# Performance work log

Measured on AMD Instinct MI355X. Metric: run time of the kernel, lower is better.

The kernel has to match this reference:

```python
import jax, jax.numpy as jnp
import numpy as np

# ---------------- geometry constants (from init_kwargs) ----------------
N_PROJ = 96          # cone-beam projections (batch of 2D BP, views of 3D BP)
A2D    = 96          # 2D parallel angles (= detector rows of cone sinogram)
DET2D  = 192         # 2D detector bins   (= detector cols of cone sinogram)
DS2D   = 1.0         # 2D detector spacing
H = 128
W = 128              # intermediate CB_projection image (geom_2d volume)
Zd = 128
Yd = 128
Xd = 128             # reconstruction volume (geometry.volume_shape)
DSO = 500.0          # source-isocenter distance
DSD = 1000.0         # source-detector distance
DU = 3.5
DV = 3.5             # 3D detector spacing (detector grid == H x W image grid)


def _grad_lastdim(x):
    # torch.gradient(x, dim=-1) with unit spacing: central diffs, one-sided edges
    left = x[..., 1:2] - x[..., 0:1]
    mid = (x[..., 2:] - x[..., :-2]) * 0.5
    right = x[..., -1:] - x[..., -2:-1]
    return jnp.concatenate([left, mid, right], axis=-1)


def _image_grid(h, w):
    ys = jnp.arange(h, dtype=jnp.float32) - (h - 1) / 2.0
    xs = jnp.arange(w, dtype=jnp.float32) - (w - 1) / 2.0
    yg, xg = jnp.meshgrid(ys, xs, indexing='ij')  # [h, w]
    return yg, xg


def _weights_3d():
    # Defrise-Clack intermediate-function weighting: cosine of ray angle,
    # w(x,y) = D / sqrt(D^2 + x^2 + y^2) on the intermediate image grid.
    yg, xg = _image_grid(H, W)
    return DSD / jnp.sqrt(DSD * DSD + xg * xg + yg * yg)


def _bp2d(sino):
    # Pixel-driven 2D parallel backprojection, batched over N.
    # sino: [N, A2D, DET2D] -> [N, H, W]
    yg, xg = _image_grid(H, W)
    th = jnp.arange(A2D, dtype=jnp.float32) * (np.pi / A2D)
    s = jnp.cos(th)[:, None, None] * xg + jnp.sin(th)[:, None, None] * yg  # [A,H,W]
    pos = s / DS2D + (DET2D - 1) / 2.0
    i0 = jnp.floor(pos).astype(jnp.int32)
    f = pos - i0
    i1 = i0 + 1
    w0 = jnp.where((i0 >= 0) & (i0 < DET2D), 1.0 - f, 0.0)
    w1 = jnp.where((i1 >= 0) & (i1 < DET2D), f, 0.0)
    i0c = jnp.clip(i0, 0, DET2D - 1)
    i1c = jnp.clip(i1, 0, DET2D - 1)
    aa = jnp.arange(A2D)[:, None, None]  # [A,1,1]
    g0 = sino[:, aa, i0c]  # [N, A, H, W]
    g1 = sino[:, aa, i1c]
    return (g0 * w0 + g1 * w1).sum(axis=1)  # [N, H, W]


def _bp3d(projs):
    # Voxel-driven circular cone-beam backprojection with FDK distance weight.
    # projs: [N_PROJ, H, W] (V=H rows, U=W cols) -> volume [Zd, Yd, Xd]
    zs = jnp.arange(Zd, dtype=jnp.float32) - (Zd - 1) / 2.0
    ys = jnp.arange(Yd, dtype=jnp.float32) - (Yd - 1) / 2.0
    xs = jnp.arange(Xd, dtype=jnp.float32) - (Xd - 1) / 2.0
    zz, yy, xx = jnp.meshgrid(zs, ys, xs, indexing='ij')  # [Z,Y,X]
    betas = jnp.arange(N_PROJ, dtype=jnp.float32) * (2.0 * np.pi / N_PROJ)

    def body(acc, inp):
        beta, proj = inp
        cb, sb = jnp.cos(beta), jnp.sin(beta)
        t = xx * cb + yy * sb          # along central ray
        s = -xx * sb + yy * cb         # transaxial offset
        r = DSO + t                    # source-to-voxel-plane distance
        pu = (DSD * s / r) / DU + (W - 1) / 2.0
        pv = (DSD * zz / r) / DV + (H - 1) / 2.0
        iu0 = jnp.floor(pu).astype(jnp.int32); fu = pu - iu0; iu1 = iu0 + 1
        iv0 = jnp.floor(pv).astype(jnp.int32); fv = pv - iv0; iv1 = iv0 + 1
        mu0 = (iu0 >= 0) & (iu0 < W); mu1 = (iu1 >= 0) & (iu1 < W)
        mv0 = (iv0 >= 0) & (iv0 < H); mv1 = (iv1 >= 0) & (iv1 < H)
        iu0c = jnp.clip(iu0, 0, W - 1); iu1c = jnp.clip(iu1, 0, W - 1)
        iv0c = jnp.clip(iv0, 0, H - 1); iv1c = jnp.clip(iv1, 0, H - 1)
        w00 = jnp.where(mv0 & mu0, (1 - fv) * (1 - fu), 0.0)
        w01 = jnp.where(mv0 & mu1, (1 - fv) * fu, 0.0)
        w10 = jnp.where(mv1 & mu0, fv * (1 - fu), 0.0)
        w11 = jnp.where(mv1 & mu1, fv * fu, 0.0)
        val = (proj[iv0c, iu0c] * w00 + proj[iv0c, iu1c] * w01 +
               proj[iv1c, iu0c] * w10 + proj[iv1c, iu1c] * w11)
        acc = acc + val * (DSD / r) ** 2
        return acc, None

    acc, _ = jax.lax.scan(body, jnp.zeros((Zd, Yd, Xd), jnp.float32), (betas, projs))
    return acc


def setup_inputs() -> dict:
    key = jax.random.key(0)
    k1, k2 = jax.random.split(key)
    sinogram = jax.random.normal(k1, (1, 1, N_PROJ, A2D, DET2D), dtype=jnp.float32)
    weight = jax.random.uniform(k2, (1, N_PROJ, A2D, DET2D), dtype=jnp.float32)
    prelu_weight = jnp.full((1,), 0.25, dtype=jnp.float32)
    return {"sinogram": sinogram, "weight": weight, "prelu_weight": prelu_weight}


def reference(sinogram, weight, prelu_weight):
    ws = sinogram[0] * weight                 # [1, N, A, D]
    deriv = _grad_lastdim(ws)[0]              # [N, A, D]  (squeeze dim 0)
    cb = _bp2d(deriv)                         # [N, H, W]
    weighted_cb = cb * _weights_3d()          # [N, H, W]
    reco = _bp3d(weighted_cb)[None]           # [1, Z, Y, X]
    a = prelu_weight[0]
    return jnp.where(reco >= 0, reco, a * reco)  # PReLU (single parameter)
```

## Files before the change

### kernel.cpp

```cpp
#include <hip/hip_runtime.h>
#include <hip/hip_fp16.h>
#include <math.h>

#define NPROJ 96
#define NANG  96
#define DET   192
#define NPIX  16384
#define SLICE (NANG*DET)

#define KPROJ 285.7142857142857f

__device__ __forceinline__ float frcp(float x) { return __builtin_amdgcn_rcpf(x); }

__device__ __forceinline__ float ffract(float x) {
#if __has_builtin(__builtin_amdgcn_fractf)
    return __builtin_amdgcn_fractf(x);
#else
    return x - floorf(x);
#endif
}

typedef __fp16 h2 __attribute__((ext_vector_type(2)));

__device__ __forceinline__ unsigned pack2(float a, float b) {
    h2 p = __builtin_amdgcn_cvt_pkrtz(a, b);
    return __builtin_bit_cast(unsigned, p);
}
__device__ __forceinline__ h2 as_h2(unsigned u) { return __builtin_bit_cast(h2, u); }

#if __has_builtin(__builtin_amdgcn_fdot2)
#define FDOT2(a, b, c) __builtin_amdgcn_fdot2((a), (b), (c), false)
#else
__device__ __forceinline__ float FDOT2(h2 a, h2 b, float c) {
    return c + (float)a[0] * (float)b[0] + (float)a[1] * (float)b[1];
}
#endif

__global__ __launch_bounds__(192) void k_deriv(const float* __restrict__ sino,
                                               const float* __restrict__ wgt,
                                               unsigned* __restrict__ derivp) {
    __shared__ float row[DET];
    const int r = blockIdx.x;
    const int d = threadIdx.x;
    const int base = r * DET + d;
    row[d] = sino[base] * wgt[base];
    __syncthreads();
    float g0, g1;
    if (d == 0)            g0 = row[1] - row[0];
    else if (d == DET-1)   g0 = row[DET-1] - row[DET-2];
    else                   g0 = 0.5f * (row[d+1] - row[d-1]);
    if (d >= DET-2)        g1 = (d == DET-1) ? 0.0f : row[DET-1] - row[DET-2];
    else                   g1 = 0.5f * (row[d+2] - row[d]);
    derivp[base] = pack2(g0, g1);
}

__global__ __launch_bounds__(256) void k_bp2d(const unsigned* __restrict__ derivp,
                                              unsigned* __restrict__ wcb4) {
    __shared__ float sc[NANG], ss[NANG];
    __shared__ float buf[512];
    const int p   = blockIdx.x;
    const int tid = threadIdx.x;

    if (tid < NANG) {
        float s_, c_;
        sincosf((float)tid * (float)(3.14159265358979323846 / 96.0), &s_, &c_);
        sc[tid] = c_; ss[tid] = s_;
    }

    const int pixbase = blockIdx.y * 512;
    float acc[2], fx[2], fy[2];
    #pragma unroll
    for (int i = 0; i < 2; ++i) {
        const int pix = pixbase + i*256 + tid;
        fx[i] = (float)(pix & 127) - 63.5f;
        fy[i] = (float)(pix >> 7)  - 63.5f;
        acc[i] = 0.0f;
    }
    __syncthreads();

    const unsigned* rowp = derivp + p * SLICE;
    for (int a = 0; a < NANG; ++a, rowp += DET) {
        const float cb = sc[a], sb = ss[a];
        #pragma unroll
        for (int i = 0; i < 2; ++i) {
            const float pos = fmaf(cb, fx[i], fmaf(sb, fy[i], 95.5f));
            const int   i0  = (int)pos;
            const float f   = ffract(pos);
            const h2    g   = as_h2(rowp[i0]);
            acc[i] = FDOT2(g, as_h2(pack2(1.0f - f, f)), acc[i]);
        }
    }

    #pragma unroll
    for (int i = 0; i < 2; ++i) {
        const float w = 1000.0f * rsqrtf(1000000.0f + fx[i]*fx[i] + fy[i]*fy[i]);
        buf[i*256 + tid] = acc[i] * w;
    }
    __syncthreads();
    unsigned* slice4 = wcb4 + p * (NPIX * 2);
    #pragma unroll
    for (int i = 0; i < 2; ++i) {
        const int l   = i*256 + tid;
        const int pix = pixbase + l;
        const int u   = pix & 127;
        const int v   = pix >> 7;
        const float v0 = buf[l];
        const float v1 = (u < 127) ? buf[l + 1] : 0.0f;
        const unsigned pr = pack2(v0, v1);
        slice4[pix * 2] = pr;
        if (v >= 1) slice4[(pix - 128) * 2 + 1] = pr;
    }
}

__global__ __launch_bounds__(256) void k_bp3d(const uint2* __restrict__ wcb4,
                                              const float* __restrict__ prelu,
                                              float* __restrict__ out) {
    __shared__ float sc[NPROJ], ss[NPROJ];
    const int tid = threadIdx.x;
    const int x   = tid & 127;
    const int y   = (blockIdx.x << 1) | (tid >> 7);
    const int z0  = blockIdx.y << 2;

    if (tid < NPROJ) {
        float s_, c_;
        sincosf((float)tid * (float)(2.0 * 3.14159265358979323846 / 96.0), &s_, &c_);
        sc[tid] = c_; ss[tid] = s_;
    }

    const float fx  = (float)x - 63.5f;
    const float fy  = (float)y - 63.5f;
    const float zlo = (float)z0 - 63.5f;

    float acc[4];
    #pragma unroll
    for (int j = 0; j < 4; ++j) acc[j] = 0.0f;

    __syncthreads();

    const uint2* bb = wcb4;
    for (int b = 0; b < NPROJ; ++b, bb += NPIX) {
        const float cb    = sc[b], sb = ss[b];
        const float t     = fmaf(fx, cb,  fy * sb);
        const float sdist = fmaf(fy, cb, -fx * sb);
        const float invr  = frcp(500.0f + t);
        const float pu    = fmaf(KPROJ * sdist, invr, 63.5f);
        const int   iu0   = (int)pu;
        const float fu    = ffract(pu);
        float w2 = 1000.0f * invr; w2 *= w2;
        const float Kz    = KPROJ * invr;
        const h2    wu    = as_h2(pack2(1.0f - fu, fu));

        int   off[4];
        float fv[4];
        #pragma unroll
        for (int j = 0; j < 4; ++j) {
            const float pv  = fmaf(Kz, zlo + (float)j, 63.5f);
            const int   iv0 = (int)pv;
            fv[j]  = ffract(pv);
            off[j] = (iv0 << 7) + iu0;
        }
        uint2 g[4];
        #pragma unroll
        for (int j = 0; j < 4; ++j) g[j] = bb[off[j]];
        #pragma unroll
        for (int j = 0; j < 4; ++j) {
            const float top = FDOT2(as_h2(g[j].x), wu, 0.0f);
            const float bot = FDOT2(as_h2(g[j].y), wu, 0.0f);
            acc[j] = fmaf(fmaf(fv[j], bot - top, top), w2, acc[j]);
        }
    }

    const float a = prelu[0];
    #pragma unroll
    for (int j = 0; j < 4; ++j) {
        const float v = acc[j];
        out[((z0 + j) << 14) + (y << 7) + x] = (v >= 0.0f) ? v : a * v;
    }
}

extern "C" void kernel_launch(void* const* d_in, const int* in_sizes, int n_in,
                              void* d_out, int out_size, void* d_ws, size_t ws_size,
                              hipStream_t stream) {
    const float* sino  = (const float*)d_in[0];
    const float* wgt   = (const float*)d_in[1];
    const float* prelu = (const float*)d_in[2];
    unsigned* derivp = (unsigned*)d_ws;
    unsigned* wcb4   = derivp + NPROJ * SLICE;
    float* out = (float*)d_out;

    k_deriv<<<dim3(NPROJ * NANG), dim3(192), 0, stream>>>(sino, wgt, derivp);
    k_bp2d <<<dim3(NPROJ, 32),    dim3(256), 0, stream>>>(derivp, wcb4);
    k_bp3d <<<dim3(64, 32),       dim3(256), 0, stream>>>((const uint2*)wcb4, prelu, out);
}
```

Measured before the change: 198.8 us.

## Pack row-pair quads for 3D backprojection and pair pixels in 2D backprojection

Changes the intermediate cone-projection layout so each 16-byte entry holds four consecutive detector rows (two row-pairs) as fp16 pairs. In the 3D backprojection two adjacent z-slices can then share one uint4 gather instead of two uint2 gathers. The 2D backprojection now has each thread handle two horizontally adjacent pixels, and the derivative kernel emits a three-sample window so both pixels read one uint2. The cost is more select logic, double the derivative workspace, and a fallback path chosen by workspace size; the layout also assumes two neighbouring z-slices land within a span of four rows.

```diff
diff --git a/kernel.cpp b/kernel.cpp
--- a/kernel.cpp
+++ b/kernel.cpp
@@ -35,6 +35,25 @@
     return c + (float)a[0] * (float)b[0] + (float)a[1] * (float)b[1];
 }
 #endif
+
+__global__ __launch_bounds__(192) void k_deriv2(const float* __restrict__ sino,
+                                                const float* __restrict__ wgt,
+                                                uint2* __restrict__ derivq) {
+    __shared__ float row[DET];
+    const int r = blockIdx.x;
+    const int d = threadIdx.x;
+    const int base = r * DET + d;
+    row[d] = sino[base] * wgt[base];
+    __syncthreads();
+    auto grad = [&](int i) -> float {
+        i = (i > DET-1) ? DET-1 : i;
+        if (i == 0)       return row[1] - row[0];
+        if (i == DET-1)   return row[DET-1] - row[DET-2];
+        return 0.5f * (row[i+1] - row[i-1]);
+    };
+    const float g0 = grad(d), g1 = grad(d+1), g2 = grad(d+2);
+    derivq[base] = make_uint2(pack2(g0, g1), pack2(g1, g2));
+}
 
 __global__ __launch_bounds__(192) void k_deriv(const float* __restrict__ sino,
                                                const float* __restrict__ wgt,
@@ -45,74 +64,114 @@
     const int base = r * DET + d;
     row[d] = sino[base] * wgt[base];
     __syncthreads();
-    float g0, g1;
-    if (d == 0)            g0 = row[1] - row[0];
-    else if (d == DET-1)   g0 = row[DET-1] - row[DET-2];
-    else                   g0 = 0.5f * (row[d+1] - row[d-1]);
-    if (d >= DET-2)        g1 = (d == DET-1) ? 0.0f : row[DET-1] - row[DET-2];
-    else                   g1 = 0.5f * (row[d+2] - row[d]);
-    derivp[base] = pack2(g0, g1);
-}
-
-__global__ __launch_bounds__(256) void k_bp2d(const unsigned* __restrict__ derivp,
-                                              unsigned* __restrict__ wcb4) {
-    __shared__ float sc[NANG], ss[NANG];
-    __shared__ float buf[512];
-    const int p   = blockIdx.x;
-    const int tid = threadIdx.x;
-
-    if (tid < NANG) {
-        float s_, c_;
-        sincosf((float)tid * (float)(3.14159265358979323846 / 96.0), &s_, &c_);
-        sc[tid] = c_; ss[tid] = s_;
-    }
-
-    const int pixbase = blockIdx.y * 512;
-    float acc[2], fx[2], fy[2];
+    auto grad = [&](int i) -> float {
+        i = (i > DET-1) ? DET-1 : i;
+        if (i == 0)       return row[1] - row[0];
+        if (i == DET-1)   return row[DET-1] - row[DET-2];
+        return 0.5f * (row[i+1] - row[i-1]);
+    };
+    derivp[base] = pack2(grad(d), grad(d+1));
+}
+
+__device__ __forceinline__ void bp2d_epilogue(float* buf, int tid, int pixbase,
+                                              int p, unsigned* wcbq_dw) {
+    __syncthreads();
+    unsigned* sq = wcbq_dw + p * 32768;
     #pragma unroll
     for (int i = 0; i < 2; ++i) {
-        const int pix = pixbase + i*256 + tid;
-        fx[i] = (float)(pix & 127) - 63.5f;
-        fy[i] = (float)(pix >> 7)  - 63.5f;
-        acc[i] = 0.0f;
-    }
-    __syncthreads();
-
-    const unsigned* rowp = derivp + p * SLICE;
-    for (int a = 0; a < NANG; ++a, rowp += DET) {
-        const float cb = sc[a], sb = ss[a];
-        #pragma unroll
-        for (int i = 0; i < 2; ++i) {
-            const float pos = fmaf(cb, fx[i], fmaf(sb, fy[i], 95.5f));
-            const int   i0  = (int)pos;
-            const float f   = ffract(pos);
-            const h2    g   = as_h2(rowp[i0]);
-            acc[i] = FDOT2(g, as_h2(pack2(1.0f - f, f)), acc[i]);
-        }
-    }
-
-    #pragma unroll
-    for (int i = 0; i < 2; ++i) {
-        const float w = 1000.0f * rsqrtf(1000000.0f + fx[i]*fx[i] + fy[i]*fy[i]);
-        buf[i*256 + tid] = acc[i] * w;
-    }
-    __syncthreads();
-    unsigned* slice4 = wcb4 + p * (NPIX * 2);
-    #pragma unroll
-    for (int i = 0; i < 2; ++i) {
-        const int l   = i*256 + tid;
+        const int l   = 2*tid + i;
         const int pix = pixbase + l;
         const int u   = pix & 127;
         const int v   = pix >> 7;
         const float v0 = buf[l];
         const float v1 = (u < 127) ? buf[l + 1] : 0.0f;
         const unsigned pr = pack2(v0, v1);
-        slice4[pix * 2] = pr;
-        if (v >= 1) slice4[(pix - 128) * 2 + 1] = pr;
-    }
-}
-
-__global__ __launch_bounds__(256) void k_bp3d(const uint2* __restrict__ wcb4,
+        const int vq1 = v >> 1, k1 = v & 1;
+        sq[(((vq1 << 7) + u) << 2) + k1] = pr;
+        const int vq2 = vq1 - 1;
+        if (vq2 >= 0) sq[(((vq2 << 7) + u) << 2) + k1 + 2] = pr;
+    }
+}
+
+__global__ __launch_bounds__(256) void k_bp2d_pair(const uint2* __restrict__ derivq,
+                                                   unsigned* __restrict__ wcbq_dw) {
+    __shared__ float sc[NANG], ss[NANG];
+    __shared__ float buf[512];
+    const int p   = blockIdx.x;
+    const int tid = threadIdx.x;
+
+    if (tid < NANG) {
+        float s_, c_;
+        sincosf((float)tid * (float)(3.14159265358979323846 / 96.0), &s_, &c_);
+        sc[tid] = c_; ss[tid] = s_;
+    }
+
+    const int pixbase = blockIdx.y * 512;
+    const int px0 = pixbase + 2*tid;
+    const float fx0 = (float)(px0 & 127) - 63.5f;
+    const float fy  = (float)(px0 >> 7)  - 63.5f;
+    float acc0 = 0.0f, acc1 = 0.0f;
+    __syncthreads();
+
+    const uint2* rowq = derivq + p * SLICE;
+    for (int a = 0; a < NANG; ++a, rowq += DET) {
+        const float cb = sc[a], sb = ss[a];
+        const float pos0 = fmaf(cb, fx0, fmaf(sb, fy, 95.5f));
+        const float pos1 = pos0 + cb;
+        const int i0 = (int)pos0;
+        const int i1 = (int)pos1;
+        const int m  = (i0 < i1) ? i0 : i1;
+        const uint2 q = rowq[m];
+        const unsigned pa = (i0 == m) ? q.x : q.y;
+        const unsigned pb = (i1 == m) ? q.x : q.y;
+        const float f0 = ffract(pos0);
+        const float f1 = ffract(pos1);
+        acc0 = FDOT2(as_h2(pa), as_h2(pack2(1.0f - f0, f0)), acc0);
+        acc1 = FDOT2(as_h2(pb), as_h2(pack2(1.0f - f1, f1)), acc1);
+    }
+
+    const float fx1 = fx0 + 1.0f;
+    buf[2*tid]     = acc0 * (1000.0f * rsqrtf(1000000.0f + fx0*fx0 + fy*fy));
+    buf[2*tid + 1] = acc1 * (1000.0f * rsqrtf(1000000.0f + fx1*fx1 + fy*fy));
+    bp2d_epilogue(buf, tid, pixbase, p, wcbq_dw);
+}
+
+__global__ __launch_bounds__(256) void k_bp2d_fb(const unsigned* __restrict__ derivp,
+                                                 unsigned* __restrict__ wcbq_dw) {
+    __shared__ float sc[NANG], ss[NANG];
+    __shared__ float buf[512];
+    const int p   = blockIdx.x;
+    const int tid = threadIdx.x;
+    if (tid < NANG) {
+        float s_, c_;
+        sincosf((float)tid * (float)(3.14159265358979323846 / 96.0), &s_, &c_);
+        sc[tid] = c_; ss[tid] = s_;
+    }
+    const int pixbase = blockIdx.y * 512;
+    const int px0 = pixbase + 2*tid;
+    const float fx0 = (float)(px0 & 127) - 63.5f;
+    const float fy  = (float)(px0 >> 7)  - 63.5f;
+    float acc0 = 0.0f, acc1 = 0.0f;
+    __syncthreads();
+    const unsigned* rowp = derivp + p * SLICE;
+    for (int a = 0; a < NANG; ++a, rowp += DET) {
+        const float cb = sc[a], sb = ss[a];
+        const float pos0 = fmaf(cb, fx0, fmaf(sb, fy, 95.5f));
+        const float pos1 = pos0 + cb;
+        const int i0 = (int)pos0;
+        const int i1 = (int)pos1;
+        const float f0 = ffract(pos0);
+        const float f1 = ffract(pos1);
+        acc0 = FDOT2(as_h2(rowp[i0]), as_h2(pack2(1.0f - f0, f0)), acc0);
+        acc1 = FDOT2(as_h2(rowp[i1]), as_h2(pack2(1.0f - f1, f1)), acc1);
+    }
+    const float fx1 = fx0 + 1.0f;
+    buf[2*tid]     = acc0 * (1000.0f * rsqrtf(1000000.0f + fx0*fx0 + fy*fy));
+    buf[2*tid + 1] = acc1 * (1000.0f * rsqrtf(1000000.0f + fx1*fx1 + fy*fy));
+    bp2d_epilogue(buf, tid, pixbase, p, wcbq_dw);
+}
+
+__global__ __launch_bounds__(256) void k_bp3d(const uint4* __restrict__ wcbq,
                                               const float* __restrict__ prelu,
                                               float* __restrict__ out) {
     __shared__ float sc[NPROJ], ss[NPROJ];
@@ -137,8 +196,8 @@
 
     __syncthreads();
 
-    const uint2* bb = wcb4;
-    for (int b = 0; b < NPROJ; ++b, bb += NPIX) {
+    const uint4* bb = wcbq;
+    for (int b = 0; b < NPROJ; ++b, bb += 8192) {
         const float cb    = sc[b], sb = ss[b];
         const float t     = fmaf(fx, cb,  fy * sb);
         const float sdist = fmaf(fy, cb, -fx * sb);
@@ -150,23 +209,28 @@
         const float Kz    = KPROJ * invr;
         const h2    wu    = as_h2(pack2(1.0f - fu, fu));
 
-        int   off[4];
-        float fv[4];
         #pragma unroll
-        for (int j = 0; j < 4; ++j) {
-            const float pv  = fmaf(Kz, zlo + (float)j, 63.5f);
-            const int   iv0 = (int)pv;
-            fv[j]  = ffract(pv);
-            off[j] = (iv0 << 7) + iu0;
-        }
-        uint2 g[4];
-        #pragma unroll
-        for (int j = 0; j < 4; ++j) g[j] = bb[off[j]];
-        #pragma unroll
-        for (int j = 0; j < 4; ++j) {
-            const float top = FDOT2(as_h2(g[j].x), wu, 0.0f);
-            const float bot = FDOT2(as_h2(g[j].y), wu, 0.0f);
-            acc[j] = fmaf(fmaf(fv[j], bot - top, top), w2, acc[j]);
+        for (int pr2 = 0; pr2 < 2; ++pr2) {
+            const float pvA = fmaf(Kz, zlo + (float)(2*pr2),     63.5f);
+            const float pvB = fmaf(Kz, zlo + (float)(2*pr2 + 1), 63.5f);
+            const int   ivA = (int)pvA;
+            const int   ivB = (int)pvB;
+            const float fvA = ffract(pvA);
+            const float fvB = ffract(pvB);
+            const int   bqi = ivA >> 1;
+            const int   s   = ivA & 1;
+            const int   dS  = ivB - (bqi << 1);
+            const uint4 q   = bb[(bqi << 7) + iu0];
+            const unsigned topA = s ? q.y : q.x;
+            const unsigned botA = s ? q.z : q.y;
+            unsigned topB = (dS >= 1) ? q.y : q.x;  topB = (dS >= 2) ? q.z : topB;
+            unsigned botB = (dS >= 1) ? q.z : q.y;  botB = (dS >= 2) ? q.w : botB;
+            const float tA = FDOT2(as_h2(topA), wu, 0.0f);
+            const float bA = FDOT2(as_h2(botA), wu, 0.0f);
+            acc[2*pr2]     = fmaf(fmaf(fvA, bA - tA, tA), w2, acc[2*pr2]);
+            const float tB = FDOT2(as_h2(topB), wu, 0.0f);
+            const float bB = FDOT2(as_h2(botB), wu, 0.0f);
+            acc[2*pr2 + 1] = fmaf(fmaf(fvB, bB - tB, tB), w2, acc[2*pr2 + 1]);
         }
     }
 
@@ -184,11 +248,19 @@
     const float* sino  = (const float*)d_in[0];
     const float* wgt   = (const float*)d_in[1];
     const float* prelu = (const float*)d_in[2];
-    unsigned* derivp = (unsigned*)d_ws;
-    unsigned* wcb4   = derivp + NPROJ * SLICE;
     float* out = (float*)d_out;
 
-    k_deriv<<<dim3(NPROJ * NANG), dim3(192), 0, stream>>>(sino, wgt, derivp);
-    k_bp2d <<<dim3(NPROJ, 32),    dim3(256), 0, stream>>>(derivp, wcb4);
-    k_bp3d <<<dim3(64, 32),       dim3(256), 0, stream>>>((const uint2*)wcb4, prelu, out);
-}
+    const size_t wcbq_bytes = (size_t)NPROJ * 64 * 128 * 16;
+    unsigned* wcbq_dw = (unsigned*)d_ws;
+    char*     deriv_p = (char*)d_ws + wcbq_bytes;
+    const size_t need_primary = wcbq_bytes + (size_t)NPROJ * SLICE * 8;
+
+    if (ws_size >= need_primary) {
+        k_deriv2<<<dim3(NPROJ * NANG), dim3(192), 0, stream>>>(sino, wgt, (uint2*)deriv_p);
+        k_bp2d_pair<<<dim3(NPROJ, 32), dim3(256), 0, stream>>>((const uint2*)deriv_p, wcbq_dw);
+    } else {
+        k_deriv<<<dim3(NPROJ * NANG), dim3(192), 0, stream>>>(sino, wgt, (unsigned*)deriv_p);
+        k_bp2d_fb<<<dim3(NPROJ, 32), dim3(256), 0, stream>>>((const unsigned*)deriv_p, wcbq_dw);
+    }
+    k_bp3d<<<dim3(64, 32), dim3(256), 0, stream>>>((const uint4*)wcbq_dw, prelu, out);
+}
```

Result: slower. 220.0 us (+10.7%).

## Store four-row packed fp16 quads so 3D backprojection fetches two z-samples per load

Applied to the files above, without the earlier changes.

The 2D backprojection now writes each intermediate pixel pair into a 4-row interleaved layout (16 bytes per texel), so one uint4 load in the 3D backprojection covers the rows needed for two adjacent z voxels. The per-projection weight w2 is folded into the packed u-interpolation weights, which removes one multiply per voxel. The quad layout doubles the intermediate buffer and its write traffic, and it assumes adjacent z samples never differ by more than one detector row. A fallback path keeps the old 2-row layout when workspace is too small.

```diff
diff --git a/kernel.cpp b/kernel.cpp
--- a/kernel.cpp
+++ b/kernel.cpp
@@ -54,8 +54,9 @@
     derivp[base] = pack2(g0, g1);
 }
 
-__global__ __launch_bounds__(256) void k_bp2d(const unsigned* __restrict__ derivp,
-                                              unsigned* __restrict__ wcb4) {
+template <int QUAD>
+__global__ __launch_bounds__(256) void k_bp2d_t(const unsigned* __restrict__ derivp,
+                                                unsigned* __restrict__ dst) {
     __shared__ float sc[NANG], ss[NANG];
     __shared__ float buf[512];
     const int p   = blockIdx.x;
@@ -97,7 +98,6 @@
         buf[i*256 + tid] = acc[i] * w;
     }
     __syncthreads();
-    unsigned* slice4 = wcb4 + p * (NPIX * 2);
     #pragma unroll
     for (int i = 0; i < 2; ++i) {
         const int l   = i*256 + tid;
@@ -107,14 +107,24 @@
         const float v0 = buf[l];
         const float v1 = (u < 127) ? buf[l + 1] : 0.0f;
         const unsigned pr = pack2(v0, v1);
-        slice4[pix * 2] = pr;
-        if (v >= 1) slice4[(pix - 128) * 2 + 1] = pr;
-    }
-}
-
-__global__ __launch_bounds__(256) void k_bp3d(const uint2* __restrict__ wcb4,
-                                              const float* __restrict__ prelu,
-                                              float* __restrict__ out) {
+        if (QUAD) {
+            unsigned* sq = dst + p * (NPIX * 4);
+            #pragma unroll
+            for (int k = 0; k < 4; ++k) {
+                const int vb = v - k;
+                if (vb >= 0) sq[(((vb << 7) + u) << 2) + k] = pr;
+            }
+        } else {
+            unsigned* s2 = dst + p * (NPIX * 2);
+            s2[pix * 2] = pr;
+            if (v >= 1) s2[(pix - 128) * 2 + 1] = pr;
+        }
+    }
+}
+
+__global__ __launch_bounds__(256) void k_bp3d_q(const uint4* __restrict__ wq,
+                                                const float* __restrict__ prelu,
+                                                float* __restrict__ out) {
     __shared__ float sc[NPROJ], ss[NPROJ];
     const int tid = threadIdx.x;
     const int x   = tid & 127;
@@ -135,6 +145,70 @@
     #pragma unroll
     for (int j = 0; j < 4; ++j) acc[j] = 0.0f;
 
+    __syncthreads();
+
+    const uint4* bb = wq;
+    for (int b = 0; b < NPROJ; ++b, bb += NPIX) {
+        const float cb    = sc[b], sb = ss[b];
+        const float t     = fmaf(fx, cb,  fy * sb);
+        const float sdist = fmaf(fy, cb, -fx * sb);
+        const float invr  = frcp(500.0f + t);
+        const float pu    = fmaf(KPROJ * sdist, invr, 63.5f);
+        const int   iu0   = (int)pu;
+        const float fu    = ffract(pu);
+        float w2 = 1000.0f * invr; w2 *= w2;
+        const float Kz    = KPROJ * invr;
+        const h2    wuw   = as_h2(pack2((1.0f - fu) * w2, fu * w2));
+
+        #pragma unroll
+        for (int pr2 = 0; pr2 < 2; ++pr2) {
+            const float pvA = fmaf(Kz, zlo + (float)(2*pr2), 63.5f);
+            const float pvB = pvA + Kz;
+            const int   ivA = (int)pvA;
+            const int   ivB = (int)pvB;
+            const float fvA = ffract(pvA);
+            const float fvB = ffract(pvB);
+            const uint4 q   = bb[(ivA << 7) + iu0];
+            const int   d   = ivB - ivA;
+            const float tA  = FDOT2(as_h2(q.x), wuw, 0.0f);
+            const float bA  = FDOT2(as_h2(q.y), wuw, 0.0f);
+            acc[2*pr2]     += fmaf(fvA, bA - tA, tA);
+            const unsigned tBv = d ? q.y : q.x;
+            const unsigned bBv = d ? q.z : q.y;
+            const float tB  = FDOT2(as_h2(tBv), wuw, 0.0f);
+            const float bB  = FDOT2(as_h2(bBv), wuw, 0.0f);
+            acc[2*pr2 + 1] += fmaf(fvB, bB - tB, tB);
+        }
+    }
+
+    const float a = prelu[0];
+    #pragma unroll
+    for (int j = 0; j < 4; ++j) {
+        const float v = acc[j];
+        out[((z0 + j) << 14) + (y << 7) + x] = (v >= 0.0f) ? v : a * v;
+    }
+}
+
+__global__ __launch_bounds__(256) void k_bp3d_fb(const uint2* __restrict__ wcb4,
+                                                 const float* __restrict__ prelu,
+                                                 float* __restrict__ out) {
+    __shared__ float sc[NPROJ], ss[NPROJ];
+    const int tid = threadIdx.x;
+    const int x   = tid & 127;
+    const int y   = (blockIdx.x << 1) | (tid >> 7);
+    const int z0  = blockIdx.y << 2;
+
+    if (tid < NPROJ) {
+        float s_, c_;
+        sincosf((float)tid * (float)(2.0 * 3.14159265358979323846 / 96.0), &s_, &c_);
+        sc[tid] = c_; ss[tid] = s_;
+    }
+    const float fx  = (float)x - 63.5f;
+    const float fy  = (float)y - 63.5f;
+    const float zlo = (float)z0 - 63.5f;
+    float acc[4];
+    #pragma unroll
+    for (int j = 0; j < 4; ++j) acc[j] = 0.0f;
     __syncthreads();
 
     const uint2* bb = wcb4;
@@ -148,8 +222,7 @@
         const float fu    = ffract(pu);
         float w2 = 1000.0f * invr; w2 *= w2;
         const float Kz    = KPROJ * invr;
-        const h2    wu    = as_h2(pack2(1.0f - fu, fu));
-
+        const h2    wuw   = as_h2(pack2((1.0f - fu) * w2, fu * w2));
         int   off[4];
         float fv[4];
         #pragma unroll
@@ -164,12 +237,11 @@
         for (int j = 0; j < 4; ++j) g[j] = bb[off[j]];
         #pragma unroll
         for (int j = 0; j < 4; ++j) {
-            const float top = FDOT2(as_h2(g[j].x), wu, 0.0f);
-            const float bot = FDOT2(as_h2(g[j].y), wu, 0.0f);
-            acc[j] = fmaf(fmaf(fv[j], bot - top, top), w2, acc[j]);
-        }
-    }
-
+            const float top = FDOT2(as_h2(g[j].x), wuw, 0.0f);
+            const float bot = FDOT2(as_h2(g[j].y), wuw, 0.0f);
+            acc[j] += fmaf(fv[j], bot - top, top);
+        }
+    }
     const float a = prelu[0];
     #pragma unroll
     for (int j = 0; j < 4; ++j) {
@@ -184,11 +256,20 @@
     const float* sino  = (const float*)d_in[0];
     const float* wgt   = (const float*)d_in[1];
     const float* prelu = (const float*)d_in[2];
+    float* out = (float*)d_out;
+
+    const size_t deriv_bytes = (size_t)NPROJ * SLICE * 4;
+    const size_t quad_bytes  = (size_t)NPROJ * NPIX * 16;
     unsigned* derivp = (unsigned*)d_ws;
-    unsigned* wcb4   = derivp + NPROJ * SLICE;
-    float* out = (float*)d_out;
+    unsigned* store  = derivp + NPROJ * SLICE;
 
     k_deriv<<<dim3(NPROJ * NANG), dim3(192), 0, stream>>>(sino, wgt, derivp);
-    k_bp2d <<<dim3(NPROJ, 32),    dim3(256), 0, stream>>>(derivp, wcb4);
-    k_bp3d <<<dim3(64, 32),       dim3(256), 0, stream>>>((const uint2*)wcb4, prelu, out);
-}
+
+    if (ws_size >= deriv_bytes + quad_bytes) {
+        k_bp2d_t<1><<<dim3(NPROJ, 32), dim3(256), 0, stream>>>(derivp, store);
+        k_bp3d_q<<<dim3(64, 32), dim3(256), 0, stream>>>((const uint4*)store, prelu, out);
+    } else {
+        k_bp2d_t<0><<<dim3(NPROJ, 32), dim3(256), 0, stream>>>(derivp, store);
+        k_bp3d_fb<<<dim3(64, 32), dim3(256), 0, stream>>>((const uint2*)store, prelu, out);
+    }
+}
```

Result: faster. 193.3 us (-2.8%).
